# Optimization experiments

Hardware: AMD Instinct MI355X
Metric: run time of the kernel (lower is better)

The kernel has to match this reference:

```python
import jax, jax.numpy as jnp
import numpy as np

B, S, H = 2, 2048, 2048
NH, NKV, HD = 16, 4, 128
THETA = 1000000.0

def _rope_tables(seq_len, dim, theta):
    inv_freq = 1.0 / (theta ** (np.arange(0, dim, 2, dtype=np.float32) / dim))
    t = np.arange(seq_len, dtype=np.float32)
    freqs = np.outer(t, inv_freq)                      # [S, dim/2]
    emb = np.concatenate([freqs, freqs], axis=-1)      # [S, dim]
    return jnp.asarray(np.cos(emb)), jnp.asarray(np.sin(emb))

def setup_inputs() -> dict:
    key = jax.random.key(0)
    ks = jax.random.split(key, 5)
    cos, sin = _rope_tables(S, HD, THETA)
    scale = 1.0 / np.sqrt(H)
    return {
        "x": jax.random.normal(ks[0], (B, S, H), jnp.float32),
        "cos": cos, "sin": sin,
        "wq": jax.random.normal(ks[1], (H, NH * HD), jnp.float32) * scale,
        "wk": jax.random.normal(ks[2], (H, NKV * HD), jnp.float32) * scale,
        "wv": jax.random.normal(ks[3], (H, NKV * HD), jnp.float32) * scale,
        "wo": jax.random.normal(ks[4], (NH * HD, H), jnp.float32) * scale,
    }

def _rotate_half(t):
    h = t.shape[-1] // 2
    return jnp.concatenate([-t[..., h:], t[..., :h]], axis=-1)

def reference(x, cos, sin, wq, wk, wv, wo):
    b, s, _ = x.shape
    n_rep = NH // NKV
    q = (x @ wq).reshape(b, s, NH, HD)    # [b,s,nh,hd]
    k = (x @ wk).reshape(b, s, NKV, HD)
    v = (x @ wv).reshape(b, s, NKV, HD)
    # RoPE: cos/sin [s,hd] broadcast over batch and heads
    c = cos[None, :, None, :]
    sn = sin[None, :, None, :]
    q = q * c + _rotate_half(q) * sn
    k = k * c + _rotate_half(k) * sn
    # GQA: repeat kv heads n_rep times
    k = jnp.repeat(k, n_rep, axis=2)      # [b,s,nh,hd]
    v = jnp.repeat(v, n_rep, axis=2)
    q = q.transpose(0, 2, 1, 3)           # [b,nh,s,hd]
    k = k.transpose(0, 2, 1, 3)
    v = v.transpose(0, 2, 1, 3)
    scores = jnp.einsum('bhqd,bhkd->bhqk', q, k) / jnp.sqrt(jnp.float32(HD))
    causal = jnp.tril(jnp.ones((s, s), dtype=bool))
    scores = jnp.where(causal[None, None], scores, jnp.float32(-jnp.inf))
    attn = jax.nn.softmax(scores.astype(jnp.float32), axis=-1).astype(q.dtype)
    out = jnp.einsum('bhqk,bhkd->bhqd', attn, v)
    out = out.transpose(0, 2, 1, 3).reshape(b, s, NH * HD)
    return out @ wo
```

## Files before the change

kernel.cpp:

```cpp
#include <hip/hip_runtime.h>
#include <hip/hip_bf16.h>

#define Bb 2
#define Ss 2048
#define Hh 2048
#define NH 16
#define NKV 4
#define HD 128
#define NREP (NH / NKV)
#define Mrows (Bb * Ss)
#define NQKV (NH*HD + 2*NKV*HD)

using short8 = __attribute__((ext_vector_type(8))) short;
using f32x4  = __attribute__((ext_vector_type(4))) float;

__device__ __forceinline__ unsigned short f2b(float f) {
  union { float f; unsigned u; } v; v.f = f;
  return (unsigned short)((v.u + 0x7fffu + ((v.u >> 16) & 1u)) >> 16);
}
__device__ __forceinline__ float b2f(unsigned short h) {
  union { unsigned u; float f; } v; v.u = ((unsigned)h) << 16; return v.f;
}

__device__ __forceinline__ void gload16(const void* g, void* l) {
  __builtin_amdgcn_global_load_lds(
      (const __attribute__((address_space(1))) unsigned int*)g,
      (__attribute__((address_space(3))) unsigned int*)l, 16, 0, 0);
}

__global__ void cvt_bf16(const float* __restrict__ in, unsigned short* __restrict__ out, int n) {
  int i = (blockIdx.x * blockDim.x + threadIdx.x) * 4;
  if (i < n) {
    float4 f = *(const float4*)(in + i);
    ushort4 o;
    o.x = f2b(f.x); o.y = f2b(f.y); o.z = f2b(f.z); o.w = f2b(f.w);
    *(ushort4*)(out + i) = o;
  }
}

__global__ void transpose_cvt(const float* __restrict__ in, unsigned short* __restrict__ out,
                              int R, int C) {
  __shared__ float tile[32][33];
  int c0 = blockIdx.x * 32, r0 = blockIdx.y * 32;
  int tx = threadIdx.x, ty = threadIdx.y;
  #pragma unroll
  for (int i = ty; i < 32; i += 8)
    tile[i][tx] = in[(long)(r0 + i) * C + c0 + tx];
  __syncthreads();
  #pragma unroll
  for (int i = ty; i < 32; i += 8)
    out[(long)(c0 + i) * R + r0 + tx] = f2b(tile[tx][i]);
}

template <bool OUT_BF16>
__global__ __launch_bounds__(256) void gemm_bt(const unsigned short* __restrict__ A,
                                               const unsigned short* __restrict__ Bt,
                                               void* __restrict__ Cv,
                                               int Mm, int Nn, int Kk) {
  __shared__ unsigned short As[128 * 32];
  __shared__ unsigned short Bs[128 * 32];
  const int t = threadIdx.x;
  const int lane = t & 63, wave = t >> 6;
  const int quad = lane >> 4, l16 = lane & 15;
  const int m0 = blockIdx.y * 128, n0 = blockIdx.x * 128;
  const int wm = (wave >> 1) * 64, wn = (wave & 1) * 64;

  f32x4 acc[4][4] = {};

  const unsigned short* Ag0 = A + (long)(m0 + (t >> 2)) * Kk + (t & 3) * 8;
  const unsigned short* Ag1 = A + (long)(m0 + 64 + (t >> 2)) * Kk + (t & 3) * 8;
  const unsigned short* Bg0 = Bt + (long)(n0 + (t >> 2)) * Kk + (t & 3) * 8;
  const unsigned short* Bg1 = Bt + (long)(n0 + 64 + (t >> 2)) * Kk + (t & 3) * 8;
  unsigned short* lA0 = As + (wave * 64) * 8;
  unsigned short* lA1 = As + (wave * 64 + 256) * 8;
  unsigned short* lB0 = Bs + (wave * 64) * 8;
  unsigned short* lB1 = Bs + (wave * 64 + 256) * 8;

  for (int k0 = 0; k0 < Kk; k0 += 32) {
    gload16(Ag0 + k0, lA0);
    gload16(Ag1 + k0, lA1);
    gload16(Bg0 + k0, lB0);
    gload16(Bg1 + k0, lB1);
    __syncthreads();

    short8 af[4], bf[4];
    #pragma unroll
    for (int i = 0; i < 4; i++)
      af[i] = *(const short8*)(As + (wm + i * 16 + l16) * 32 + quad * 8);
    #pragma unroll
    for (int i = 0; i < 4; i++)
      bf[i] = *(const short8*)(Bs + (wn + i * 16 + l16) * 32 + quad * 8);

    #pragma unroll
    for (int mi = 0; mi < 4; mi++)
      #pragma unroll
      for (int ni = 0; ni < 4; ni++)
        acc[mi][ni] = __builtin_amdgcn_mfma_f32_16x16x32_bf16(af[mi], bf[ni], acc[mi][ni], 0, 0, 0);
    __syncthreads();
  }

  #pragma unroll
  for (int mi = 0; mi < 4; mi++)
    #pragma unroll
    for (int ni = 0; ni < 4; ni++)
      #pragma unroll
      for (int r = 0; r < 4; r++) {
        long row = m0 + wm + mi * 16 + quad * 4 + r;
        long col = n0 + wn + ni * 16 + l16;
        if (OUT_BF16)
          ((unsigned short*)Cv)[row * Nn + col] = f2b(acc[mi][ni][r]);
        else
          ((float*)Cv)[row * Nn + col] = acc[mi][ni][r];
      }
}

__global__ void rope_reshape(const unsigned short* __restrict__ qkv,
                             const float* __restrict__ cosT, const float* __restrict__ sinT,
                             unsigned short* __restrict__ qt, unsigned short* __restrict__ kt,
                             unsigned short* __restrict__ vt) {
  int row = blockIdx.x;
  int b = row / Ss, s = row % Ss;
  const unsigned short* r = qkv + (long)row * NQKV;
  for (int i = threadIdx.x; i < NQKV; i += blockDim.x) {
    if (i < NH * HD) {
      int h = i / HD, d = i % HD;
      float val = b2f(r[i]);
      float partner = b2f(r[h * HD + ((d < 64) ? d + 64 : d - 64)]);
      float c = cosT[s * HD + d], sn = sinT[s * HD + d];
      float o = val * c + ((d < 64) ? -partner : partner) * sn;
      qt[(((long)b * NH + h) * Ss + s) * HD + d] = f2b(o);
    } else if (i < NH * HD + NKV * HD) {
      int j = i - NH * HD;
      int h = j / HD, d = j % HD;
      float val = b2f(r[i]);
      float partner = b2f(r[NH * HD + h * HD + ((d < 64) ? d + 64 : d - 64)]);
      float c = cosT[s * HD + d], sn = sinT[s * HD + d];
      float o = val * c + ((d < 64) ? -partner : partner) * sn;
      kt[(((long)b * NKV + h) * Ss + s) * HD + d] = f2b(o);
    } else {
      int j = i - NH * HD - NKV * HD;
      int h = j / HD, d = j % HD;
      vt[(((long)b * NKV + h) * HD + d) * Ss + s] = r[i];
    }
  }
}

__global__ __launch_bounds__(256, 2) void flash_attn(const unsigned short* __restrict__ qt,
                                                     const unsigned short* __restrict__ kt,
                                                     const unsigned short* __restrict__ vt,
                                                     unsigned short* __restrict__ out) {
  __shared__ unsigned short Ks[2][64 * 128];
  __shared__ unsigned short Vs[2][128 * 64];
  __shared__ unsigned short Ps[4][16 * 72];

  const int w = threadIdx.x >> 6, lane = threadIdx.x & 63;
  const int quad = lane >> 4, l16 = lane & 15;
  const int idx = blockIdx.x;
  const int qblk = (Ss / 64) - 1 - (idx >> 5);
  const int bh = idx & 31;
  const int h = bh & (NH - 1), b = bh >> 4;
  const int q0 = qblk * 64 + w * 16;
  const int kvh = h / NREP;

  const unsigned short* Qb = qt + ((long)b * NH + h) * Ss * HD;
  const unsigned short* Kb = kt + ((long)b * NKV + kvh) * Ss * HD;
  const unsigned short* Vb = vt + ((long)b * NKV + kvh) * HD * Ss;
  unsigned short* Pw = Ps[w];

  const int nch = qblk + 1;
  const int r8 = lane >> 3, c8 = lane & 7;

  {
    #pragma unroll
    for (int i = 0; i < 4; i++) {
      int r = i * 16 + w * 4 + quad;
      int sg = l16 ^ (w * 4 + quad);
      gload16(Kb + (long)r * HD + sg * 8, &Ks[0][(i * 256 + w * 64) * 8]);
    }
    #pragma unroll
    for (int i = 0; i < 4; i++) {
      int r = i * 32 + w * 8 + r8;
      int sg = c8 ^ r8;
      gload16(Vb + (long)r * Ss + sg * 8, &Vs[0][(i * 256 + w * 64) * 8]);
    }
  }

  short8 aq[4];
  #pragma unroll
  for (int kc = 0; kc < 4; kc++)
    aq[kc] = *(const short8*)(Qb + (long)(q0 + l16) * HD + kc * 32 + quad * 8);

  f32x4 accO[8] = {};
  float m_i[4], l_i[4];
  #pragma unroll
  for (int r = 0; r < 4; r++) { m_i[r] = -__builtin_inff(); l_i[r] = 0.f; }
  const float cscale = 1.4426950408889634f * 0.08838834764831845f;

  for (int c = 0; c < nch; ++c) {
    const unsigned short* Ksb = Ks[c & 1];
    const unsigned short* Vsb = Vs[c & 1];

    if (c + 1 < nch) {
      const int k0 = (c + 1) * 64;
      unsigned short* Kd = Ks[(c + 1) & 1];
      unsigned short* Vd = Vs[(c + 1) & 1];
      #pragma unroll
      for (int i = 0; i < 4; i++) {
        int r = i * 16 + w * 4 + quad;
        int sg = l16 ^ (w * 4 + quad);
        gload16(Kb + (long)(k0 + r) * HD + sg * 8, Kd + (i * 256 + w * 64) * 8);
      }
      #pragma unroll
      for (int i = 0; i < 4; i++) {
        int r = i * 32 + w * 8 + r8;
        int sg = c8 ^ r8;
        gload16(Vb + (long)r * Ss + k0 + sg * 8, Vd + (i * 256 + w * 64) * 8);
      }
      asm volatile("s_waitcnt vmcnt(8)" ::: "memory");
    } else {
      asm volatile("s_waitcnt vmcnt(0)" ::: "memory");
    }
    asm volatile("s_barrier" ::: "memory");

    f32x4 sc[4] = {};
    #pragma unroll
    for (int kc = 0; kc < 4; kc++)
      #pragma unroll
      for (int nt = 0; nt < 4; nt++) {
        short8 bk = *(const short8*)(Ksb + ((nt * 16 + l16) * 16 + ((kc * 4 + quad) ^ l16)) * 8);
        sc[nt] = __builtin_amdgcn_mfma_f32_16x16x32_bf16(aq[kc], bk, sc[nt], 0, 0, 0);
      }

    if (c == nch - 1) {
      #pragma unroll
      for (int nt = 0; nt < 4; nt++) {
        int kj = c * 64 + nt * 16 + l16;
        #pragma unroll
        for (int r = 0; r < 4; r++)
          if (kj > q0 + quad * 4 + r) sc[nt][r] = -__builtin_inff();
      }
    }

    float mx[4];
    #pragma unroll
    for (int r = 0; r < 4; r++) {
      float v = fmaxf(fmaxf(sc[0][r], sc[1][r]), fmaxf(sc[2][r], sc[3][r]));
      v = fmaxf(v, __shfl_xor(v, 1));
      v = fmaxf(v, __shfl_xor(v, 2));
      v = fmaxf(v, __shfl_xor(v, 4));
      v = fmaxf(v, __shfl_xor(v, 8));
      mx[r] = v;
    }
    float rsum[4];
    #pragma unroll
    for (int r = 0; r < 4; r++) {
      float mn = fmaxf(m_i[r], mx[r]);
      float alpha = __builtin_amdgcn_exp2f((m_i[r] - mn) * cscale);
      m_i[r] = mn;
      l_i[r] *= alpha;
      #pragma unroll
      for (int nt = 0; nt < 8; nt++) accO[nt][r] *= alpha;
      rsum[r] = 0.f;
      #pragma unroll
      for (int nt = 0; nt < 4; nt++) {
        float p = __builtin_amdgcn_exp2f((sc[nt][r] - mn) * cscale);
        rsum[r] += p;
        Pw[(quad * 4 + r) * 72 + nt * 16 + l16] = f2b(p);
      }
    }
    #pragma unroll
    for (int r = 0; r < 4; r++) {
      float v = rsum[r];
      v += __shfl_xor(v, 1);
      v += __shfl_xor(v, 2);
      v += __shfl_xor(v, 4);
      v += __shfl_xor(v, 8);
      l_i[r] += v;
    }

    short8 ap0 = *(const short8*)(Pw + l16 * 72 + quad * 8);
    short8 ap1 = *(const short8*)(Pw + l16 * 72 + 32 + quad * 8);
    #pragma unroll
    for (int nt = 0; nt < 8; nt++) {
      short8 bv0 = *(const short8*)(Vsb + ((nt * 16 + l16) * 8 + (quad ^ c8 ^ (r8 & 1) * 0 ^ (l16 & 7) ^ c8 ^ (l16 & 7) * 0)) * 8);
      (void)bv0;
      break;
    }
    #pragma unroll
    for (int nt = 0; nt < 8; nt++) {
      short8 bv0 = *(const short8*)(Vsb + ((nt * 16 + l16) * 8 + (quad ^ (l16 & 7))) * 8);
      short8 bv1 = *(const short8*)(Vsb + ((nt * 16 + l16) * 8 + ((4 + quad) ^ (l16 & 7))) * 8);
      accO[nt] = __builtin_amdgcn_mfma_f32_16x16x32_bf16(ap0, bv0, accO[nt], 0, 0, 0);
      accO[nt] = __builtin_amdgcn_mfma_f32_16x16x32_bf16(ap1, bv1, accO[nt], 0, 0, 0);
    }

    asm volatile("s_waitcnt lgkmcnt(0)" ::: "memory");
    asm volatile("s_barrier" ::: "memory");
  }

  #pragma unroll
  for (int r = 0; r < 4; r++) {
    float inv = 1.f / l_i[r];
    long orow = (long)b * Ss + q0 + quad * 4 + r;
    #pragma unroll
    for (int nt = 0; nt < 8; nt++)
      out[orow * (NH * HD) + h * HD + nt * 16 + l16] = f2b(accO[nt][r] * inv);
  }
}

extern "C" void kernel_launch(void* const* d_in, const int* in_sizes, int n_in,
                              void* d_out, int out_size, void* d_ws, size_t ws_size,
                              hipStream_t stream) {
  const float* x   = (const float*)d_in[0];
  const float* cosT = (const float*)d_in[1];
  const float* sinT = (const float*)d_in[2];
  const float* wq  = (const float*)d_in[3];
  const float* wk  = (const float*)d_in[4];
  const float* wv  = (const float*)d_in[5];
  const float* wo  = (const float*)d_in[6];
  float* out = (float*)d_out;

  char* ws = (char*)d_ws;
  unsigned short* xb    = (unsigned short*)(ws + 0);
  unsigned short* wqkvt = (unsigned short*)(ws + 16777216);
  unsigned short* wot   = (unsigned short*)(ws + 29360128);
  unsigned short* qkv   = (unsigned short*)(ws + 37748736);
  unsigned short* kt    = (unsigned short*)(ws + 62914560);
  unsigned short* vt    = (unsigned short*)(ws + 67108864);
  unsigned short* qt    = xb;
  unsigned short* attno = qkv;

  cvt_bf16<<<Mrows * Hh / 4 / 256, 256, 0, stream>>>(x, xb, Mrows * Hh);

  dim3 tb(32, 8);
  transpose_cvt<<<dim3(Hh / 32, Hh / 32), tb, 0, stream>>>(wq, wqkvt, Hh, NH * HD);
  transpose_cvt<<<dim3(NKV * HD / 32, Hh / 32), tb, 0, stream>>>(wk, wqkvt + (long)NH * HD * Hh, Hh, NKV * HD);
  transpose_cvt<<<dim3(NKV * HD / 32, Hh / 32), tb, 0, stream>>>(wv, wqkvt + (long)(NH * HD + NKV * HD) * Hh, Hh, NKV * HD);
  transpose_cvt<<<dim3(Hh / 32, Hh / 32), tb, 0, stream>>>(wo, wot, Hh, Hh);

  gemm_bt<true><<<dim3(NQKV / 128, Mrows / 128), 256, 0, stream>>>(xb, wqkvt, qkv, Mrows, NQKV, Hh);

  rope_reshape<<<Mrows, 256, 0, stream>>>(qkv, cosT, sinT, qt, kt, vt);

  flash_attn<<<(Ss / 64) * NH * Bb, 256, 0, stream>>>(qt, kt, vt, attno);

  gemm_bt<false><<<dim3(Hh / 128, Mrows / 128), 256, 0, stream>>>(attno, wot, out, Mrows, Hh, Hh);
}
```

Measured before the change: 365.3 us.

## Enlarge attention Q tile, keep P in registers, split RoPE and V transpose

Flash attention now processes 128 query rows per block, with two 16-row tiles per wave. Each K/V fragment read from LDS is reused across both query tiles. S is computed transposed (K as the A operand) and the key order is permuted so the P fragments can be fed straight into the PV MFMA from registers, which removes the LDS round trip for P. The grid order pairs heavy and light query blocks, chunks lying entirely above the diagonal are skipped, and outputs are stored as vectors. RoPE is rewritten to handle both halves per thread, and the V transpose moves into a separate tiled LDS transpose kernel that replaces the strided scatter; this adds one launch and raises register pressure.

```diff
diff --git a/kernel.cpp b/kernel.cpp
--- a/kernel.cpp
+++ b/kernel.cpp
@@ -114,35 +114,41 @@
       }
 }
 
-__global__ void rope_reshape(const unsigned short* __restrict__ qkv,
-                             const float* __restrict__ cosT, const float* __restrict__ sinT,
-                             unsigned short* __restrict__ qt, unsigned short* __restrict__ kt,
-                             unsigned short* __restrict__ vt) {
+__global__ void rope_qk(const unsigned short* __restrict__ qkv,
+                        const float* __restrict__ cosT, const float* __restrict__ sinT,
+                        unsigned short* __restrict__ qt, unsigned short* __restrict__ kt) {
   int row = blockIdx.x;
-  int b = row / Ss, s = row % Ss;
+  int b = row >> 11, s = row & (Ss - 1);
   const unsigned short* r = qkv + (long)row * NQKV;
-  for (int i = threadIdx.x; i < NQKV; i += blockDim.x) {
-    if (i < NH * HD) {
-      int h = i / HD, d = i % HD;
-      float val = b2f(r[i]);
-      float partner = b2f(r[h * HD + ((d < 64) ? d + 64 : d - 64)]);
-      float c = cosT[s * HD + d], sn = sinT[s * HD + d];
-      float o = val * c + ((d < 64) ? -partner : partner) * sn;
-      qt[(((long)b * NH + h) * Ss + s) * HD + d] = f2b(o);
-    } else if (i < NH * HD + NKV * HD) {
-      int j = i - NH * HD;
-      int h = j / HD, d = j % HD;
-      float val = b2f(r[i]);
-      float partner = b2f(r[NH * HD + h * HD + ((d < 64) ? d + 64 : d - 64)]);
-      float c = cosT[s * HD + d], sn = sinT[s * HD + d];
-      float o = val * c + ((d < 64) ? -partner : partner) * sn;
-      kt[(((long)b * NKV + h) * Ss + s) * HD + d] = f2b(o);
+  for (int jj = threadIdx.x; jj < (NH + NKV) * 64; jj += 256) {
+    int hh = jj >> 6, d = jj & 63;
+    float c = cosT[s * HD + d], sn = sinT[s * HD + d];
+    float x0 = b2f(r[hh * 128 + d]), x1 = b2f(r[hh * 128 + 64 + d]);
+    float o0 = x0 * c - x1 * sn;
+    float o1 = x1 * c + x0 * sn;
+    if (hh < NH) {
+      unsigned short* dst = qt + (((long)b * NH + hh) * Ss + s) * HD + d;
+      dst[0] = f2b(o0); dst[64] = f2b(o1);
     } else {
-      int j = i - NH * HD - NKV * HD;
-      int h = j / HD, d = j % HD;
-      vt[(((long)b * NKV + h) * HD + d) * Ss + s] = r[i];
+      unsigned short* dst = kt + (((long)b * NKV + (hh - NH)) * Ss + s) * HD + d;
+      dst[0] = f2b(o0); dst[64] = f2b(o1);
     }
   }
+}
+
+__global__ void vtrans(const unsigned short* __restrict__ qkv, unsigned short* __restrict__ vt) {
+  __shared__ unsigned short tile[32][33];
+  int bh = blockIdx.z;
+  int b = bh >> 2, kvh = bh & 3;
+  int d0 = blockIdx.y * 32, s0 = blockIdx.x * 32;
+  int tx = threadIdx.x, ty = threadIdx.y;
+  #pragma unroll
+  for (int i = ty; i < 32; i += 8)
+    tile[i][tx] = qkv[(long)(b * Ss + s0 + i) * NQKV + (NH + NKV) * HD + kvh * HD + d0 + tx];
+  __syncthreads();
+  #pragma unroll
+  for (int i = ty; i < 32; i += 8)
+    vt[((long)bh * HD + d0 + i) * Ss + s0 + tx] = tile[tx][i];
 }
 
 __global__ __launch_bounds__(256, 2) void flash_attn(const unsigned short* __restrict__ qt,
@@ -151,49 +157,48 @@
                                                      unsigned short* __restrict__ out) {
   __shared__ unsigned short Ks[2][64 * 128];
   __shared__ unsigned short Vs[2][128 * 64];
-  __shared__ unsigned short Ps[4][16 * 72];
 
   const int w = threadIdx.x >> 6, lane = threadIdx.x & 63;
   const int quad = lane >> 4, l16 = lane & 15;
+  const int r8 = lane >> 3, c8 = lane & 7;
   const int idx = blockIdx.x;
-  const int qblk = (Ss / 64) - 1 - (idx >> 5);
+  const int t5 = idx >> 5;
+  const int qblk = (idx < 256) ? (15 - t5) : (t5 - 8);
   const int bh = idx & 31;
   const int h = bh & (NH - 1), b = bh >> 4;
-  const int q0 = qblk * 64 + w * 16;
+  const int q0w = qblk * 128 + w * 32;
   const int kvh = h / NREP;
 
   const unsigned short* Qb = qt + ((long)b * NH + h) * Ss * HD;
   const unsigned short* Kb = kt + ((long)b * NKV + kvh) * Ss * HD;
   const unsigned short* Vb = vt + ((long)b * NKV + kvh) * HD * Ss;
-  unsigned short* Pw = Ps[w];
-
-  const int nch = qblk + 1;
-  const int r8 = lane >> 3, c8 = lane & 7;
-
-  {
-    #pragma unroll
-    for (int i = 0; i < 4; i++) {
-      int r = i * 16 + w * 4 + quad;
-      int sg = l16 ^ (w * 4 + quad);
-      gload16(Kb + (long)r * HD + sg * 8, &Ks[0][(i * 256 + w * 64) * 8]);
-    }
-    #pragma unroll
-    for (int i = 0; i < 4; i++) {
-      int r = i * 32 + w * 8 + r8;
-      int sg = c8 ^ r8;
-      gload16(Vb + (long)r * Ss + sg * 8, &Vs[0][(i * 256 + w * 64) * 8]);
-    }
-  }
-
-  short8 aq[4];
-  #pragma unroll
-  for (int kc = 0; kc < 4; kc++)
-    aq[kc] = *(const short8*)(Qb + (long)(q0 + l16) * HD + kc * 32 + quad * 8);
-
-  f32x4 accO[8] = {};
-  float m_i[4], l_i[4];
-  #pragma unroll
-  for (int r = 0; r < 4; r++) { m_i[r] = -__builtin_inff(); l_i[r] = 0.f; }
+  const int nch = (qblk + 1) * 2;
+
+  #pragma unroll
+  for (int i = 0; i < 4; i++) {
+    int rho = i * 16 + w * 4 + quad;
+    int key = (rho & 32) + ((rho >> 2) & 3) * 8 + ((rho >> 4) & 1) * 4 + (rho & 3);
+    int sg = l16 ^ (w * 4 + quad);
+    gload16(Kb + (long)key * HD + sg * 8, &Ks[0][(i * 256 + w * 64) * 8]);
+  }
+  #pragma unroll
+  for (int i = 0; i < 4; i++) {
+    int dv = i * 32 + w * 8 + r8;
+    int sg = c8 ^ r8;
+    gload16(Vb + (long)dv * Ss + sg * 8, &Vs[0][(i * 256 + w * 64) * 8]);
+  }
+
+  short8 qf[2][4];
+  #pragma unroll
+  for (int qi = 0; qi < 2; qi++)
+    #pragma unroll
+    for (int kc = 0; kc < 4; kc++)
+      qf[qi][kc] = *(const short8*)(Qb + (long)(q0w + qi * 16 + l16) * HD + kc * 32 + quad * 8);
+
+  f32x4 accO[2][8] = {};
+  float m_i[2], l_i[2];
+  m_i[0] = m_i[1] = -__builtin_inff();
+  l_i[0] = l_i[1] = 0.f;
   const float cscale = 1.4426950408889634f * 0.08838834764831845f;
 
   for (int c = 0; c < nch; ++c) {
@@ -206,15 +211,16 @@
       unsigned short* Vd = Vs[(c + 1) & 1];
       #pragma unroll
       for (int i = 0; i < 4; i++) {
-        int r = i * 16 + w * 4 + quad;
+        int rho = i * 16 + w * 4 + quad;
+        int key = (rho & 32) + ((rho >> 2) & 3) * 8 + ((rho >> 4) & 1) * 4 + (rho & 3);
         int sg = l16 ^ (w * 4 + quad);
-        gload16(Kb + (long)(k0 + r) * HD + sg * 8, Kd + (i * 256 + w * 64) * 8);
+        gload16(Kb + (long)(k0 + key) * HD + sg * 8, Kd + (i * 256 + w * 64) * 8);
       }
       #pragma unroll
       for (int i = 0; i < 4; i++) {
-        int r = i * 32 + w * 8 + r8;
+        int dv = i * 32 + w * 8 + r8;
         int sg = c8 ^ r8;
-        gload16(Vb + (long)r * Ss + k0 + sg * 8, Vd + (i * 256 + w * 64) * 8);
+        gload16(Vb + (long)dv * Ss + k0 + sg * 8, Vd + (i * 256 + w * 64) * 8);
       }
       asm volatile("s_waitcnt vmcnt(8)" ::: "memory");
     } else {
@@ -222,76 +228,83 @@
     }
     asm volatile("s_barrier" ::: "memory");
 
-    f32x4 sc[4] = {};
-    #pragma unroll
-    for (int kc = 0; kc < 4; kc++)
-      #pragma unroll
-      for (int nt = 0; nt < 4; nt++) {
-        short8 bk = *(const short8*)(Ksb + ((nt * 16 + l16) * 16 + ((kc * 4 + quad) ^ l16)) * 8);
-        sc[nt] = __builtin_amdgcn_mfma_f32_16x16x32_bf16(aq[kc], bk, sc[nt], 0, 0, 0);
-      }
-
-    if (c == nch - 1) {
-      #pragma unroll
-      for (int nt = 0; nt < 4; nt++) {
-        int kj = c * 64 + nt * 16 + l16;
-        #pragma unroll
-        for (int r = 0; r < 4; r++)
-          if (kj > q0 + quad * 4 + r) sc[nt][r] = -__builtin_inff();
-      }
-    }
-
-    float mx[4];
-    #pragma unroll
-    for (int r = 0; r < 4; r++) {
-      float v = fmaxf(fmaxf(sc[0][r], sc[1][r]), fmaxf(sc[2][r], sc[3][r]));
-      v = fmaxf(v, __shfl_xor(v, 1));
-      v = fmaxf(v, __shfl_xor(v, 2));
-      v = fmaxf(v, __shfl_xor(v, 4));
-      v = fmaxf(v, __shfl_xor(v, 8));
-      mx[r] = v;
-    }
-    float rsum[4];
-    #pragma unroll
-    for (int r = 0; r < 4; r++) {
-      float mn = fmaxf(m_i[r], mx[r]);
-      float alpha = __builtin_amdgcn_exp2f((m_i[r] - mn) * cscale);
-      m_i[r] = mn;
-      l_i[r] *= alpha;
-      #pragma unroll
-      for (int nt = 0; nt < 8; nt++) accO[nt][r] *= alpha;
-      rsum[r] = 0.f;
-      #pragma unroll
-      for (int nt = 0; nt < 4; nt++) {
-        float p = __builtin_amdgcn_exp2f((sc[nt][r] - mn) * cscale);
-        rsum[r] += p;
-        Pw[(quad * 4 + r) * 72 + nt * 16 + l16] = f2b(p);
-      }
-    }
-    #pragma unroll
-    for (int r = 0; r < 4; r++) {
-      float v = rsum[r];
-      v += __shfl_xor(v, 1);
-      v += __shfl_xor(v, 2);
-      v += __shfl_xor(v, 4);
-      v += __shfl_xor(v, 8);
-      l_i[r] += v;
-    }
-
-    short8 ap0 = *(const short8*)(Pw + l16 * 72 + quad * 8);
-    short8 ap1 = *(const short8*)(Pw + l16 * 72 + 32 + quad * 8);
-    #pragma unroll
-    for (int nt = 0; nt < 8; nt++) {
-      short8 bv0 = *(const short8*)(Vsb + ((nt * 16 + l16) * 8 + (quad ^ c8 ^ (r8 & 1) * 0 ^ (l16 & 7) ^ c8 ^ (l16 & 7) * 0)) * 8);
-      (void)bv0;
-      break;
-    }
-    #pragma unroll
-    for (int nt = 0; nt < 8; nt++) {
-      short8 bv0 = *(const short8*)(Vsb + ((nt * 16 + l16) * 8 + (quad ^ (l16 & 7))) * 8);
-      short8 bv1 = *(const short8*)(Vsb + ((nt * 16 + l16) * 8 + ((4 + quad) ^ (l16 & 7))) * 8);
-      accO[nt] = __builtin_amdgcn_mfma_f32_16x16x32_bf16(ap0, bv0, accO[nt], 0, 0, 0);
-      accO[nt] = __builtin_amdgcn_mfma_f32_16x16x32_bf16(ap1, bv1, accO[nt], 0, 0, 0);
+    if (c * 64 < q0w + 32) {
+      f32x4 sc[2][4] = {};
+      #pragma unroll
+      for (int T = 0; T < 4; T++)
+        #pragma unroll
+        for (int kc = 0; kc < 4; kc++) {
+          short8 kf = *(const short8*)(Ksb + ((16 * T + l16) * 16 + ((kc * 4 + quad) ^ l16)) * 8);
+          #pragma unroll
+          for (int qi = 0; qi < 2; qi++)
+            sc[qi][T] = __builtin_amdgcn_mfma_f32_16x16x32_bf16(kf, qf[qi][kc], sc[qi][T], 0, 0, 0);
+        }
+
+      if ((c + 1) * 64 - 1 > q0w) {
+        #pragma unroll
+        for (int qi = 0; qi < 2; qi++) {
+          int qq = q0w + qi * 16 + l16;
+          #pragma unroll
+          for (int T = 0; T < 4; T++)
+            #pragma unroll
+            for (int r = 0; r < 4; r++) {
+              int ka = c * 64 + (T >> 1) * 32 + quad * 8 + (T & 1) * 4 + r;
+              if (ka > qq) sc[qi][T][r] = -__builtin_inff();
+            }
+        }
+      }
+
+      short8 pf[2][2];
+      #pragma unroll
+      for (int qi = 0; qi < 2; qi++) {
+        float v = sc[qi][0][0];
+        #pragma unroll
+        for (int T = 0; T < 4; T++)
+          #pragma unroll
+          for (int r = 0; r < 4; r++) v = fmaxf(v, sc[qi][T][r]);
+        v = fmaxf(v, __shfl_xor(v, 16));
+        v = fmaxf(v, __shfl_xor(v, 32));
+        float mn = fmaxf(m_i[qi], v);
+        float alpha = __builtin_amdgcn_exp2f((m_i[qi] - mn) * cscale);
+        m_i[qi] = mn;
+        l_i[qi] *= alpha;
+        #pragma unroll
+        for (int Dt = 0; Dt < 8; Dt++)
+          #pragma unroll
+          for (int r = 0; r < 4; r++) accO[qi][Dt][r] *= alpha;
+
+        float p[4][4], rs = 0.f;
+        #pragma unroll
+        for (int T = 0; T < 4; T++)
+          #pragma unroll
+          for (int r = 0; r < 4; r++) {
+            p[T][r] = __builtin_amdgcn_exp2f((sc[qi][T][r] - mn) * cscale);
+            rs += p[T][r];
+          }
+        rs += __shfl_xor(rs, 16);
+        rs += __shfl_xor(rs, 32);
+        l_i[qi] += rs;
+
+        #pragma unroll
+        for (int c2 = 0; c2 < 2; c2++) {
+          short8 f;
+          f[0] = (short)f2b(p[2 * c2][0]);     f[1] = (short)f2b(p[2 * c2][1]);
+          f[2] = (short)f2b(p[2 * c2][2]);     f[3] = (short)f2b(p[2 * c2][3]);
+          f[4] = (short)f2b(p[2 * c2 + 1][0]); f[5] = (short)f2b(p[2 * c2 + 1][1]);
+          f[6] = (short)f2b(p[2 * c2 + 1][2]); f[7] = (short)f2b(p[2 * c2 + 1][3]);
+          pf[qi][c2] = f;
+        }
+      }
+
+      #pragma unroll
+      for (int c2 = 0; c2 < 2; c2++)
+        #pragma unroll
+        for (int Dt = 0; Dt < 8; Dt++) {
+          short8 vf = *(const short8*)(Vsb + ((16 * Dt + l16) * 8 + ((4 * c2 + quad) ^ (l16 & 7))) * 8);
+          #pragma unroll
+          for (int qi = 0; qi < 2; qi++)
+            accO[qi][Dt] = __builtin_amdgcn_mfma_f32_16x16x32_bf16(vf, pf[qi][c2], accO[qi][Dt], 0, 0, 0);
+        }
     }
 
     asm volatile("s_waitcnt lgkmcnt(0)" ::: "memory");
@@ -299,12 +312,18 @@
   }
 
   #pragma unroll
-  for (int r = 0; r < 4; r++) {
-    float inv = 1.f / l_i[r];
-    long orow = (long)b * Ss + q0 + quad * 4 + r;
-    #pragma unroll
-    for (int nt = 0; nt < 8; nt++)
-      out[orow * (NH * HD) + h * HD + nt * 16 + l16] = f2b(accO[nt][r] * inv);
+  for (int qi = 0; qi < 2; qi++) {
+    float inv = 1.f / l_i[qi];
+    long orow = (long)b * Ss + q0w + qi * 16 + l16;
+    #pragma unroll
+    for (int Dt = 0; Dt < 8; Dt++) {
+      ushort4 o;
+      o.x = f2b(accO[qi][Dt][0] * inv);
+      o.y = f2b(accO[qi][Dt][1] * inv);
+      o.z = f2b(accO[qi][Dt][2] * inv);
+      o.w = f2b(accO[qi][Dt][3] * inv);
+      *(ushort4*)(out + orow * (NH * HD) + h * HD + Dt * 16 + quad * 4) = o;
+    }
   }
 }
 
@@ -327,7 +346,7 @@
   unsigned short* qkv   = (unsigned short*)(ws + 37748736);
   unsigned short* kt    = (unsigned short*)(ws + 62914560);
   unsigned short* vt    = (unsigned short*)(ws + 67108864);
-  unsigned short* qt    = xb;
+  unsigned short* qtp   = xb;
   unsigned short* attno = qkv;
 
   cvt_bf16<<<Mrows * Hh / 4 / 256, 256, 0, stream>>>(x, xb, Mrows * Hh);
@@ -340,9 +359,10 @@
 
   gemm_bt<true><<<dim3(NQKV / 128, Mrows / 128), 256, 0, stream>>>(xb, wqkvt, qkv, Mrows, NQKV, Hh);
 
-  rope_reshape<<<Mrows, 256, 0, stream>>>(qkv, cosT, sinT, qt, kt, vt);
-
-  flash_attn<<<(Ss / 64) * NH * Bb, 256, 0, stream>>>(qt, kt, vt, attno);
+  rope_qk<<<Mrows, 256, 0, stream>>>(qkv, cosT, sinT, qtp, kt);
+  vtrans<<<dim3(Ss / 32, HD / 32, Bb * NKV), tb, 0, stream>>>(qkv, vt);
+
+  flash_attn<<<(Ss / 128) * NH * Bb, 256, 0, stream>>>(qtp, kt, vt, attno);
 
   gemm_bt<false><<<dim3(Hh / 128, Mrows / 128), 256, 0, stream>>>(attno, wot, out, Mrows, Hh, Hh);
 }
```

After: 343.4 us. 1.06x faster.
